# Performance work log

Hardware: AMD Instinct MI355X
Metric: run time of the kernel (lower is better)

The kernel has to match this reference:

```python
import jax, jax.numpy as jnp
import numpy as np

N_NODES = 50000
BETA = 0.5
NEG_SLOPE = 0.2


def gat_conv(x, src, dst, W, a_src, a_dst, b):
    """Single-head GAT-style conv: gather, attend, softmax-per-dst, scatter-sum."""
    h = x @ W                                   # [N, F]
    as_ = h @ a_src                             # [N]
    ad_ = h @ a_dst                             # [N]
    e = jax.nn.leaky_relu(as_[src] + ad_[dst], NEG_SLOPE)  # [E]
    # numerically stable softmax over incoming edges of each dst node
    m = jax.ops.segment_max(e, dst, num_segments=N_NODES)  # [N]
    ex = jnp.exp(e - m[dst])                    # [E]
    denom = jax.ops.segment_sum(ex, dst, num_segments=N_NODES)  # [N]
    w = ex / denom[dst]                         # [E]
    out = jax.ops.segment_sum(w[:, None] * h[src], dst, num_segments=N_NODES)
    return out + b


def setup_inputs() -> dict:
    key = jax.random.key(0)
    ks = jax.random.split(key, 8)
    F_in, F_out = 64, 64
    x = jax.random.normal(ks[0], (N_NODES, F_in), dtype=jnp.float32)
    edge_index = jax.random.randint(ks[1], (2, 1600000), 0, N_NODES, dtype=jnp.int64)
    W = jax.random.normal(ks[2], (F_in, F_in), dtype=jnp.float32) * (1.0 / np.sqrt(F_in))
    a_src = jax.random.normal(ks[3], (F_in,), dtype=jnp.float32) * (1.0 / np.sqrt(F_in))
    a_dst = jax.random.normal(ks[4], (F_in,), dtype=jnp.float32) * (1.0 / np.sqrt(F_in))
    b = jnp.zeros((F_in,), dtype=jnp.float32)
    fc_w = jax.random.normal(ks[5], (F_in, F_out), dtype=jnp.float32) * (1.0 / np.sqrt(F_in))
    fc_b = jnp.zeros((F_out,), dtype=jnp.float32)
    return {"x": x, "edge_index": edge_index, "W": W, "a_src": a_src,
            "a_dst": a_dst, "b": b, "fc_w": fc_w, "fc_b": fc_b}


def reference(x, edge_index, W, a_src, a_dst, b, fc_w, fc_b):
    src, dst = edge_index[0], edge_index[1]
    x1 = BETA * gat_conv(x, src, dst, W, a_src, a_dst, b) + (1.0 - BETA) * x
    x2 = BETA * gat_conv(x1, src, dst, W, a_src, a_dst, b) + (1.0 - BETA) * x
    x3 = BETA * gat_conv(x2, src, dst, W, a_src, a_dst, b) + (1.0 - BETA) * x
    h = x3
    out = x3 @ fc_w + fc_b
    return (out, h)
```

## Files before the change

### kernel.cpp

```cpp
#include <hip/hip_runtime.h>
#include <hip/hip_bf16.h>
#include <math.h>

#define N_NODES 50000
#define FDIM 64
#define BETA 0.5f
#define NEG_SLOPE 0.2f

typedef __attribute__((ext_vector_type(8))) short bf16x8;
typedef __attribute__((ext_vector_type(4))) float f32x4;

__device__ __forceinline__ unsigned short f2bf(float f) {
    unsigned u = __float_as_uint(f);
    unsigned r = (u + 0x7FFFu + ((u >> 16) & 1u)) >> 16;
    return (unsigned short)r;
}
__device__ __forceinline__ float bf2f(unsigned short s) {
    return __uint_as_float((unsigned)s << 16);
}

#define CHUNK 2048
__global__ __launch_bounds__(256) void scatter_pairs(
    const unsigned int* __restrict__ eiu, const int* __restrict__ ei32,
    const long long* __restrict__ ei64, int* __restrict__ gCursor,
    unsigned int* __restrict__ pairs, int E, int CAP) {
    __shared__ int det;
    __shared__ int hist[256], base[256], cur[256];
    int t = threadIdx.x;
    if (t == 0) det = 0;
    hist[t] = 0; cur[t] = 0;
    __syncthreads();
    int beg = blockIdx.x * CHUNK;
    int end = min(E, beg + CHUNK);
    {
        int idx = beg + t;
        if (idx < E && eiu[2 * idx + 1] != 0u) atomicOr(&det, 1);
    }
    __syncthreads();
    bool is32 = det != 0;
    for (int i = beg + t; i < end; i += 256) {
        int d = is32 ? ei32[E + i] : (int)ei64[E + i];
        atomicAdd(&hist[d >> 8], 1);
    }
    __syncthreads();
    if (hist[t] > 0) base[t] = t * CAP + atomicAdd(&gCursor[t], hist[t]);
    __syncthreads();
    for (int i = beg + t; i < end; i += 256) {
        int s, d;
        if (is32) { s = ei32[i]; d = ei32[E + i]; }
        else      { s = (int)ei64[i]; d = (int)ei64[E + i]; }
        int b = d >> 8;
        int pos = base[b] + atomicAdd(&cur[b], 1);
        pairs[pos] = (unsigned int)s | ((unsigned int)(d & 255) << 16);
    }
}

__global__ __launch_bounds__(1024) void bucket_sort(
    const unsigned int* __restrict__ pairs, const int* __restrict__ gCursor,
    int* __restrict__ offsets, int* __restrict__ srcs, int N, int E, int CAP) {
    __shared__ int scb[256], cnt[256], sc[256], cur[256];
    int b = blockIdx.x, t = threadIdx.x;
    if (t < 256) scb[t] = gCursor[t];
    __syncthreads();
    for (int off = 1; off < 256; off <<= 1) {
        int v = (t < 256 && t >= off) ? scb[t - off] : 0;
        __syncthreads();
        if (t < 256) scb[t] += v;
        __syncthreads();
    }
    int cntb = gCursor[b];
    int beg = scb[b] - cntb;
    int pbase = b * CAP;
    if (b == 0 && t == 0) offsets[N] = E;
    if (t < 256) cnt[t] = 0;
    __syncthreads();
    for (int i = t; i < cntb; i += 1024) atomicAdd(&cnt[(pairs[pbase + i] >> 16) & 255u], 1);
    __syncthreads();
    if (t < 256) sc[t] = cnt[t];
    __syncthreads();
    for (int off = 1; off < 256; off <<= 1) {
        int v = (t < 256 && t >= off) ? sc[t - off] : 0;
        __syncthreads();
        if (t < 256) sc[t] += v;
        __syncthreads();
    }
    if (t < 256) {
        int excl = sc[t] - cnt[t];
        int node = (b << 8) + t;
        if (node < N) offsets[node] = beg + excl;
        cur[t] = beg + excl;
    }
    __syncthreads();
    for (int i = t; i < cntb; i += 1024) {
        unsigned int p = pairs[pbase + i];
        int pos = atomicAdd(&cur[(p >> 16) & 255u], 1);
        srcs[pos] = (int)(p & 0xFFFFu);
    }
}

__global__ __launch_bounds__(256) void prep_weights(
    const float* __restrict__ W, const float* __restrict__ fcw,
    unsigned short* __restrict__ WTh, unsigned short* __restrict__ WTl,
    unsigned short* __restrict__ FTh, unsigned short* __restrict__ FTl) {
    for (int idx = blockIdx.x * 256 + threadIdx.x; idx < 4096; idx += gridDim.x * 256) {
        int k = idx >> 6, f = idx & 63;
        float w = W[idx];
        unsigned short hi = f2bf(w);
        WTh[f * 64 + k] = hi;
        WTl[f * 64 + k] = f2bf(w - bf2f(hi));
        float w2 = fcw[idx];
        unsigned short hi2 = f2bf(w2);
        FTh[f * 64 + k] = hi2;
        FTl[f * 64 + k] = f2bf(w2 - bf2f(hi2));
    }
}

__global__ __launch_bounds__(256, 4) void transform_mfma(
    const float* __restrict__ x,
    const unsigned short* __restrict__ WTh, const unsigned short* __restrict__ WTl,
    const float* __restrict__ a_src, const float* __restrict__ a_dst,
    const float* __restrict__ bias,
    unsigned short* __restrict__ hb,
    float* __restrict__ fout,
    float* __restrict__ as_, float* __restrict__ ad_, int N) {
    __shared__ __align__(16) unsigned short WThs[64 * 72];
    __shared__ __align__(16) unsigned short WTls[64 * 72];
    int tid = threadIdx.x;
    {
        int row = tid >> 2;
        int ch = (tid & 3) * 16;
        uint4 h0 = ((const uint4*)(WTh + row * 64 + ch))[0];
        uint4 h1 = ((const uint4*)(WTh + row * 64 + ch))[1];
        uint4 l0 = ((const uint4*)(WTl + row * 64 + ch))[0];
        uint4 l1 = ((const uint4*)(WTl + row * 64 + ch))[1];
        *((uint4*)(WThs + row * 72 + ch)) = h0;
        *((uint4*)(WThs + row * 72 + ch + 8)) = h1;
        *((uint4*)(WTls + row * 72 + ch)) = l0;
        *((uint4*)(WTls + row * 72 + ch + 8)) = l1;
    }

    int wid = tid >> 6;
    int lane = tid & 63;
    int col = lane & 15;
    int quad = lane >> 4;
    int mbase = blockIdx.x * 64 + wid * 16;

    bf16x8 Ah[2], Al[2];
    int arow = mbase + col;
    const float* xr = x + (size_t)(arow < N ? arow : 0) * FDIM + quad * 8;
#pragma unroll
    for (int ks = 0; ks < 2; ks++) {
        float4 xa = *(const float4*)(xr + ks * 32);
        float4 xb = *(const float4*)(xr + ks * 32 + 4);
        float xv[8] = {xa.x, xa.y, xa.z, xa.w, xb.x, xb.y, xb.z, xb.w};
#pragma unroll
        for (int e = 0; e < 8; e++) {
            unsigned short hi = f2bf(xv[e]);
            Ah[ks][e] = (short)hi;
            Al[ks][e] = (short)f2bf(xv[e] - bf2f(hi));
        }
    }
    __syncthreads();

    f32x4 acc[4];
#pragma unroll
    for (int ft = 0; ft < 4; ft++) acc[ft] = (f32x4){0.f, 0.f, 0.f, 0.f};

#pragma unroll
    for (int ft = 0; ft < 4; ft++) {
        int f = ft * 16 + col;
#pragma unroll
        for (int ks = 0; ks < 2; ks++) {
            int off = f * 72 + ks * 32 + quad * 8;
            bf16x8 Bh = *(const bf16x8*)(WThs + off);
            bf16x8 Bl = *(const bf16x8*)(WTls + off);
            acc[ft] = __builtin_amdgcn_mfma_f32_16x16x32_bf16(Ah[ks], Bh, acc[ft], 0, 0, 0);
            acc[ft] = __builtin_amdgcn_mfma_f32_16x16x32_bf16(Ah[ks], Bl, acc[ft], 0, 0, 0);
            acc[ft] = __builtin_amdgcn_mfma_f32_16x16x32_bf16(Al[ks], Bh, acc[ft], 0, 0, 0);
        }
    }

    if (fout) {
#pragma unroll
        for (int ft = 0; ft < 4; ft++) {
            int f = ft * 16 + col;
            float bv = bias ? bias[f] : 0.f;
#pragma unroll
            for (int r = 0; r < 4; r++) {
                int node = mbase + quad * 4 + r;
                if (node < N) fout[(size_t)node * FDIM + f] = acc[ft][r] + bv;
            }
        }
    }
    if (hb) {
#pragma unroll
        for (int ft = 0; ft < 4; ft++) {
            int f = ft * 16 + col;
#pragma unroll
            for (int r = 0; r < 4; r++) {
                int node = mbase + quad * 4 + r;
                if (node < N) hb[(size_t)node * FDIM + f] = f2bf(acc[ft][r]);
            }
        }
    }
    if (as_) {
        float asv[4], adv[4];
#pragma unroll
        for (int ft = 0; ft < 4; ft++) {
            asv[ft] = a_src[ft * 16 + col];
            adv[ft] = a_dst[ft * 16 + col];
        }
#pragma unroll
        for (int r = 0; r < 4; r++) {
            float pa = 0.f, pd = 0.f;
#pragma unroll
            for (int ft = 0; ft < 4; ft++) {
                pa = fmaf(acc[ft][r], asv[ft], pa);
                pd = fmaf(acc[ft][r], adv[ft], pd);
            }
#pragma unroll
            for (int off = 1; off <= 8; off <<= 1) {
                pa += __shfl_xor(pa, off, 64);
                pd += __shfl_xor(pd, off, 64);
            }
            int node = mbase + quad * 4 + r;
            if (col == 0 && node < N) { as_[node] = pa; ad_[node] = pd; }
        }
    }
}

__global__ __launch_bounds__(256) void gat_gather(
    const unsigned short* __restrict__ hb,
    const float* __restrict__ as_, const float* __restrict__ ad_,
    const int* __restrict__ offsets, const int* __restrict__ srcs,
    const float* __restrict__ bvec, const float* __restrict__ x0,
    float* __restrict__ xout, int N) {
    int wid = (blockIdx.x * blockDim.x + threadIdx.x) >> 6;
    if (wid >= N) return;
    int lane = threadIdx.x & 63;
    int q = lane & 7;
    int eslot = lane >> 3;
    int beg = offsets[wid], end = offsets[wid + 1];
    float adv = ad_[wid];

    float acc[8];
#pragma unroll
    for (int k = 0; k < 8; k++) acc[k] = 0.f;
    float denom = 0.f;
    const unsigned short* hq = hb + (q << 3);

#define FMA8(EX, HV)                                                         \
    {                                                                        \
        acc[0] = fmaf(EX, __uint_as_float((HV).x << 16), acc[0]);            \
        acc[1] = fmaf(EX, __uint_as_float((HV).x & 0xFFFF0000u), acc[1]);    \
        acc[2] = fmaf(EX, __uint_as_float((HV).y << 16), acc[2]);            \
        acc[3] = fmaf(EX, __uint_as_float((HV).y & 0xFFFF0000u), acc[3]);    \
        acc[4] = fmaf(EX, __uint_as_float((HV).z << 16), acc[4]);            \
        acc[5] = fmaf(EX, __uint_as_float((HV).z & 0xFFFF0000u), acc[5]);    \
        acc[6] = fmaf(EX, __uint_as_float((HV).w << 16), acc[6]);            \
        acc[7] = fmaf(EX, __uint_as_float((HV).w & 0xFFFF0000u), acc[7]);    \
    }
#define LRELU_EXP(E_) __expf((E_) > 0.f ? (E_) : NEG_SLOPE * (E_))

    int i = beg + eslot;
    for (; i + 24 < end; i += 32) {
        int s0 = srcs[i];
        int s1 = srcs[i + 8];
        int s2 = srcs[i + 16];
        int s3 = srcs[i + 24];
        uint4 hv0 = *(const uint4*)(hq + ((size_t)s0 << 6));
        uint4 hv1 = *(const uint4*)(hq + ((size_t)s1 << 6));
        uint4 hv2 = *(const uint4*)(hq + ((size_t)s2 << 6));
        uint4 hv3 = *(const uint4*)(hq + ((size_t)s3 << 6));
        float e0 = as_[s0] + adv;
        float e1 = as_[s1] + adv;
        float e2 = as_[s2] + adv;
        float e3 = as_[s3] + adv;
        float ex0 = LRELU_EXP(e0);
        float ex1 = LRELU_EXP(e1);
        float ex2 = LRELU_EXP(e2);
        float ex3 = LRELU_EXP(e3);
        denom += (ex0 + ex1) + (ex2 + ex3);
        FMA8(ex0, hv0);
        FMA8(ex1, hv1);
        FMA8(ex2, hv2);
        FMA8(ex3, hv3);
    }
    for (; i < end; i += 8) {
        int s0 = srcs[i];
        uint4 hv0 = *(const uint4*)(hq + ((size_t)s0 << 6));
        float e0 = as_[s0] + adv;
        float ex0 = LRELU_EXP(e0);
        denom += ex0;
        FMA8(ex0, hv0);
    }
#undef FMA8
#undef LRELU_EXP

#pragma unroll
    for (int off = 8; off <= 32; off <<= 1) {
        denom += __shfl_xor(denom, off, 64);
#pragma unroll
        for (int k = 0; k < 8; k++) acc[k] += __shfl_xor(acc[k], off, 64);
    }
    if (lane < 8) {
        float inv = denom > 0.f ? 1.f / denom : 0.f;
        int fb = lane * 8;
        f32x4 b0 = *(const f32x4*)(bvec + fb);
        f32x4 b1 = *(const f32x4*)(bvec + fb + 4);
        f32x4 x0a = *(const f32x4*)(x0 + (size_t)wid * FDIM + fb);
        f32x4 x0b = *(const f32x4*)(x0 + (size_t)wid * FDIM + fb + 4);
        f32x4 o0, o1;
        o0.x = BETA * (acc[0] * inv + b0.x) + (1.f - BETA) * x0a.x;
        o0.y = BETA * (acc[1] * inv + b0.y) + (1.f - BETA) * x0a.y;
        o0.z = BETA * (acc[2] * inv + b0.z) + (1.f - BETA) * x0a.z;
        o0.w = BETA * (acc[3] * inv + b0.w) + (1.f - BETA) * x0a.w;
        o1.x = BETA * (acc[4] * inv + b1.x) + (1.f - BETA) * x0b.x;
        o1.y = BETA * (acc[5] * inv + b1.y) + (1.f - BETA) * x0b.y;
        o1.z = BETA * (acc[6] * inv + b1.z) + (1.f - BETA) * x0b.z;
        o1.w = BETA * (acc[7] * inv + b1.w) + (1.f - BETA) * x0b.w;
        *(f32x4*)(xout + (size_t)wid * FDIM + fb) = o0;
        *(f32x4*)(xout + (size_t)wid * FDIM + fb + 4) = o1;
    }
}

extern "C" void kernel_launch(void* const* d_in, const int* in_sizes, int n_in,
                              void* d_out, int out_size, void* d_ws, size_t ws_size,
                              hipStream_t stream) {
    const int N = N_NODES;
    const int E = in_sizes[1] / 2;
    const int NB = (N + 255) >> 8;
    const int CAP = (((E / N) * 256) * 2 + 1023) & ~1023;

    const float* x     = (const float*)d_in[0];
    const void*  ei    = d_in[1];
    const float* W     = (const float*)d_in[2];
    const float* a_src = (const float*)d_in[3];
    const float* a_dst = (const float*)d_in[4];
    const float* bvec  = (const float*)d_in[5];
    const float* fc_w  = (const float*)d_in[6];
    const float* fc_b  = (const float*)d_in[7];

    float* out = (float*)d_out;
    float* x3  = out + (size_t)N * FDIM;

    char* p = (char*)d_ws;
    auto alloc = [&](size_t bytes) -> void* {
        void* r = (void*)p;
        p += (bytes + 255) & ~(size_t)255;
        return r;
    };
    int*            gCursor  = (int*)alloc(256 * 4);
    unsigned int*   pairs    = (unsigned int*)alloc((size_t)256 * CAP * 4);
    int*            srcs     = (int*)alloc((size_t)E * 4);
    int*            offsets  = (int*)alloc((size_t)(N + 1) * 4);
    float*          as_      = (float*)alloc((size_t)N * 4);
    float*          ad_      = (float*)alloc((size_t)N * 4);
    unsigned short* hbuf     = (unsigned short*)alloc((size_t)N * FDIM * 2);
    float*          xbuf     = (float*)alloc((size_t)N * FDIM * 4);
    unsigned short* WTh      = (unsigned short*)alloc(4096 * 2);
    unsigned short* WTl      = (unsigned short*)alloc(4096 * 2);
    unsigned short* FTh      = (unsigned short*)alloc(4096 * 2);
    unsigned short* FTl      = (unsigned short*)alloc(4096 * 2);

    hipMemsetAsync(gCursor, 0, 256 * 4, stream);

    prep_weights<<<16, 256, 0, stream>>>(W, fc_w, WTh, WTl, FTh, FTl);

    scatter_pairs<<<(E + CHUNK - 1) / CHUNK, 256, 0, stream>>>(
        (const unsigned int*)ei, (const int*)ei, (const long long*)ei,
        gCursor, pairs, E, CAP);
    bucket_sort<<<NB, 1024, 0, stream>>>(pairs, gCursor, offsets, srcs, N, E, CAP);

    int tgrid = (N + 63) / 64;
    int ggrid = (N * 64 + 255) / 256;

    transform_mfma<<<tgrid, 256, 0, stream>>>(x, WTh, WTl, a_src, a_dst, nullptr,
                                              hbuf, nullptr, as_, ad_, N);
    gat_gather<<<ggrid, 256, 0, stream>>>(hbuf, as_, ad_, offsets, srcs, bvec, x, xbuf, N);
    transform_mfma<<<tgrid, 256, 0, stream>>>(xbuf, WTh, WTl, a_src, a_dst, nullptr,
                                              hbuf, nullptr, as_, ad_, N);
    gat_gather<<<ggrid, 256, 0, stream>>>(hbuf, as_, ad_, offsets, srcs, bvec, x, xbuf, N);
    transform_mfma<<<tgrid, 256, 0, stream>>>(xbuf, WTh, WTl, a_src, a_dst, nullptr,
                                              hbuf, nullptr, as_, ad_, N);
    gat_gather<<<ggrid, 256, 0, stream>>>(hbuf, as_, ad_, offsets, srcs, bvec, x, x3, N);
    transform_mfma<<<tgrid, 256, 0, stream>>>(x3, FTh, FTl, nullptr, nullptr, fc_b,
                                              nullptr, out, nullptr, nullptr, N);
}
```

Before: 265.5 us.

## Split gather into two source-range passes for cache locality of h rows

```diff
diff --git a/kernel.cpp b/kernel.cpp
--- a/kernel.cpp
+++ b/kernel.cpp
@@ -6,6 +6,7 @@
 #define FDIM 64
 #define BETA 0.5f
 #define NEG_SLOPE 0.2f
+#define HALF_SPLIT 25000
 
 typedef __attribute__((ext_vector_type(8))) short bf16x8;
 typedef __attribute__((ext_vector_type(4))) float f32x4;
@@ -17,6 +18,12 @@
 }
 __device__ __forceinline__ float bf2f(unsigned short s) {
     return __uint_as_float((unsigned)s << 16);
+}
+__device__ __forceinline__ void nt_store4(float* p, f32x4 v) {
+    __builtin_nontemporal_store(v, (f32x4*)p);
+}
+__device__ __forceinline__ f32x4 nt_load4(const float* p) {
+    return __builtin_nontemporal_load((const f32x4*)p);
 }
 
 #define CHUNK 2048
@@ -57,8 +64,9 @@
 
 __global__ __launch_bounds__(1024) void bucket_sort(
     const unsigned int* __restrict__ pairs, const int* __restrict__ gCursor,
-    int* __restrict__ offsets, int* __restrict__ srcs, int N, int E, int CAP) {
-    __shared__ int scb[256], cnt[256], sc[256], cur[256];
+    int* __restrict__ off2, int* __restrict__ srcs, int N, int E, int CAP) {
+    __shared__ int scb[256];
+    __shared__ int cnt[512], sc[512], cur[512];
     int b = blockIdx.x, t = threadIdx.x;
     if (t < 256) scb[t] = gCursor[t];
     __syncthreads();
@@ -71,30 +79,36 @@
     int cntb = gCursor[b];
     int beg = scb[b] - cntb;
     int pbase = b * CAP;
-    if (b == 0 && t == 0) offsets[N] = E;
-    if (t < 256) cnt[t] = 0;
-    __syncthreads();
-    for (int i = t; i < cntb; i += 1024) atomicAdd(&cnt[(pairs[pbase + i] >> 16) & 255u], 1);
-    __syncthreads();
-    if (t < 256) sc[t] = cnt[t];
-    __syncthreads();
-    for (int off = 1; off < 256; off <<= 1) {
-        int v = (t < 256 && t >= off) ? sc[t - off] : 0;
-        __syncthreads();
-        if (t < 256) sc[t] += v;
-        __syncthreads();
-    }
-    if (t < 256) {
-        int excl = sc[t] - cnt[t];
-        int node = (b << 8) + t;
-        if (node < N) offsets[node] = beg + excl;
-        cur[t] = beg + excl;
-    }
+    if (b == 0 && t == 0) off2[2 * N] = E;
+    if (t < 512) cnt[t] = 0;
     __syncthreads();
     for (int i = t; i < cntb; i += 1024) {
         unsigned int p = pairs[pbase + i];
-        int pos = atomicAdd(&cur[(p >> 16) & 255u], 1);
-        srcs[pos] = (int)(p & 0xFFFFu);
+        int key = (int)(((p >> 16) & 255u) << 1) | ((p & 0xFFFFu) >= HALF_SPLIT ? 1 : 0);
+        atomicAdd(&cnt[key], 1);
+    }
+    __syncthreads();
+    if (t < 512) sc[t] = cnt[t];
+    __syncthreads();
+    for (int off = 1; off < 512; off <<= 1) {
+        int v = (t < 512 && t >= off) ? sc[t - off] : 0;
+        __syncthreads();
+        if (t < 512) sc[t] += v;
+        __syncthreads();
+    }
+    if (t < 512) {
+        int excl = sc[t] - cnt[t];
+        int node = (b << 8) + (t >> 1);
+        if (node < N) off2[2 * node + (t & 1)] = beg + excl;
+        cur[t] = beg + excl;
+    }
+    __syncthreads();
+    for (int i = t; i < cntb; i += 1024) {
+        unsigned int p = pairs[pbase + i];
+        int s = (int)(p & 0xFFFFu);
+        int key = (int)(((p >> 16) & 255u) << 1) | (s >= HALF_SPLIT ? 1 : 0);
+        int pos = atomicAdd(&cur[key], 1);
+        srcs[pos] = s;
     }
 }
 
@@ -229,10 +243,23 @@
     }
 }
 
-__global__ __launch_bounds__(256) void gat_gather(
+__device__ __forceinline__ void fma8(float* acc, float ex, const uint4& hv) {
+    acc[0] = fmaf(ex, __uint_as_float(hv.x << 16), acc[0]);
+    acc[1] = fmaf(ex, __uint_as_float(hv.x & 0xFFFF0000u), acc[1]);
+    acc[2] = fmaf(ex, __uint_as_float(hv.y << 16), acc[2]);
+    acc[3] = fmaf(ex, __uint_as_float(hv.y & 0xFFFF0000u), acc[3]);
+    acc[4] = fmaf(ex, __uint_as_float(hv.z << 16), acc[4]);
+    acc[5] = fmaf(ex, __uint_as_float(hv.z & 0xFFFF0000u), acc[5]);
+    acc[6] = fmaf(ex, __uint_as_float(hv.w << 16), acc[6]);
+    acc[7] = fmaf(ex, __uint_as_float(hv.w & 0xFFFF0000u), acc[7]);
+}
+
+template <int PASS>
+__global__ __launch_bounds__(256) void gat_gather_pass(
     const unsigned short* __restrict__ hb,
     const float* __restrict__ as_, const float* __restrict__ ad_,
-    const int* __restrict__ offsets, const int* __restrict__ srcs,
+    const int* __restrict__ off2, const int* __restrict__ srcs,
+    float* __restrict__ accT, float* __restrict__ denT,
     const float* __restrict__ bvec, const float* __restrict__ x0,
     float* __restrict__ xout, int N) {
     int wid = (blockIdx.x * blockDim.x + threadIdx.x) >> 6;
@@ -240,7 +267,14 @@
     int lane = threadIdx.x & 63;
     int q = lane & 7;
     int eslot = lane >> 3;
-    int beg = offsets[wid], end = offsets[wid + 1];
+    int beg, end;
+    if (PASS == 0) {
+        int2 be = *(const int2*)(off2 + 2 * wid);
+        beg = be.x; end = be.y;
+    } else {
+        beg = off2[2 * wid + 1];
+        end = off2[2 * wid + 2];
+    }
     float adv = ad_[wid];
 
     float acc[8];
@@ -249,17 +283,6 @@
     float denom = 0.f;
     const unsigned short* hq = hb + (q << 3);
 
-#define FMA8(EX, HV)                                                         \
-    {                                                                        \
-        acc[0] = fmaf(EX, __uint_as_float((HV).x << 16), acc[0]);            \
-        acc[1] = fmaf(EX, __uint_as_float((HV).x & 0xFFFF0000u), acc[1]);    \
-        acc[2] = fmaf(EX, __uint_as_float((HV).y << 16), acc[2]);            \
-        acc[3] = fmaf(EX, __uint_as_float((HV).y & 0xFFFF0000u), acc[3]);    \
-        acc[4] = fmaf(EX, __uint_as_float((HV).z << 16), acc[4]);            \
-        acc[5] = fmaf(EX, __uint_as_float((HV).z & 0xFFFF0000u), acc[5]);    \
-        acc[6] = fmaf(EX, __uint_as_float((HV).w << 16), acc[6]);            \
-        acc[7] = fmaf(EX, __uint_as_float((HV).w & 0xFFFF0000u), acc[7]);    \
-    }
 #define LRELU_EXP(E_) __expf((E_) > 0.f ? (E_) : NEG_SLOPE * (E_))
 
     int i = beg + eslot;
@@ -281,10 +304,23 @@
         float ex2 = LRELU_EXP(e2);
         float ex3 = LRELU_EXP(e3);
         denom += (ex0 + ex1) + (ex2 + ex3);
-        FMA8(ex0, hv0);
-        FMA8(ex1, hv1);
-        FMA8(ex2, hv2);
-        FMA8(ex3, hv3);
+        fma8(acc, ex0, hv0);
+        fma8(acc, ex1, hv1);
+        fma8(acc, ex2, hv2);
+        fma8(acc, ex3, hv3);
+    }
+    for (; i + 8 < end; i += 16) {
+        int s0 = srcs[i];
+        int s1 = srcs[i + 8];
+        uint4 hv0 = *(const uint4*)(hq + ((size_t)s0 << 6));
+        uint4 hv1 = *(const uint4*)(hq + ((size_t)s1 << 6));
+        float e0 = as_[s0] + adv;
+        float e1 = as_[s1] + adv;
+        float ex0 = LRELU_EXP(e0);
+        float ex1 = LRELU_EXP(e1);
+        denom += ex0 + ex1;
+        fma8(acc, ex0, hv0);
+        fma8(acc, ex1, hv1);
     }
     for (; i < end; i += 8) {
         int s0 = srcs[i];
@@ -292,9 +328,8 @@
         float e0 = as_[s0] + adv;
         float ex0 = LRELU_EXP(e0);
         denom += ex0;
-        FMA8(ex0, hv0);
-    }
-#undef FMA8
+        fma8(acc, ex0, hv0);
+    }
 #undef LRELU_EXP
 
 #pragma unroll
@@ -303,24 +338,39 @@
 #pragma unroll
         for (int k = 0; k < 8; k++) acc[k] += __shfl_xor(acc[k], off, 64);
     }
-    if (lane < 8) {
-        float inv = denom > 0.f ? 1.f / denom : 0.f;
-        int fb = lane * 8;
-        f32x4 b0 = *(const f32x4*)(bvec + fb);
-        f32x4 b1 = *(const f32x4*)(bvec + fb + 4);
-        f32x4 x0a = *(const f32x4*)(x0 + (size_t)wid * FDIM + fb);
-        f32x4 x0b = *(const f32x4*)(x0 + (size_t)wid * FDIM + fb + 4);
-        f32x4 o0, o1;
-        o0.x = BETA * (acc[0] * inv + b0.x) + (1.f - BETA) * x0a.x;
-        o0.y = BETA * (acc[1] * inv + b0.y) + (1.f - BETA) * x0a.y;
-        o0.z = BETA * (acc[2] * inv + b0.z) + (1.f - BETA) * x0a.z;
-        o0.w = BETA * (acc[3] * inv + b0.w) + (1.f - BETA) * x0a.w;
-        o1.x = BETA * (acc[4] * inv + b1.x) + (1.f - BETA) * x0b.x;
-        o1.y = BETA * (acc[5] * inv + b1.y) + (1.f - BETA) * x0b.y;
-        o1.z = BETA * (acc[6] * inv + b1.z) + (1.f - BETA) * x0b.z;
-        o1.w = BETA * (acc[7] * inv + b1.w) + (1.f - BETA) * x0b.w;
-        *(f32x4*)(xout + (size_t)wid * FDIM + fb) = o0;
-        *(f32x4*)(xout + (size_t)wid * FDIM + fb + 4) = o1;
+
+    if (PASS == 0) {
+        if (lane < 8) {
+            int fb = lane * 8;
+            f32x4 a0 = {acc[0], acc[1], acc[2], acc[3]};
+            f32x4 a1 = {acc[4], acc[5], acc[6], acc[7]};
+            nt_store4(accT + (size_t)wid * FDIM + fb, a0);
+            nt_store4(accT + (size_t)wid * FDIM + fb + 4, a1);
+        }
+        if (lane == 0) denT[wid] = denom;
+    } else {
+        if (lane < 8) {
+            float dtot = denom + denT[wid];
+            float inv = dtot > 0.f ? 1.f / dtot : 0.f;
+            int fb = lane * 8;
+            f32x4 pa0 = nt_load4(accT + (size_t)wid * FDIM + fb);
+            f32x4 pa1 = nt_load4(accT + (size_t)wid * FDIM + fb + 4);
+            f32x4 b0 = *(const f32x4*)(bvec + fb);
+            f32x4 b1 = *(const f32x4*)(bvec + fb + 4);
+            f32x4 x0a = nt_load4(x0 + (size_t)wid * FDIM + fb);
+            f32x4 x0b = nt_load4(x0 + (size_t)wid * FDIM + fb + 4);
+            f32x4 o0, o1;
+            o0.x = BETA * ((acc[0] + pa0.x) * inv + b0.x) + (1.f - BETA) * x0a.x;
+            o0.y = BETA * ((acc[1] + pa0.y) * inv + b0.y) + (1.f - BETA) * x0a.y;
+            o0.z = BETA * ((acc[2] + pa0.z) * inv + b0.z) + (1.f - BETA) * x0a.z;
+            o0.w = BETA * ((acc[3] + pa0.w) * inv + b0.w) + (1.f - BETA) * x0a.w;
+            o1.x = BETA * ((acc[4] + pa1.x) * inv + b1.x) + (1.f - BETA) * x0b.x;
+            o1.y = BETA * ((acc[5] + pa1.y) * inv + b1.y) + (1.f - BETA) * x0b.y;
+            o1.z = BETA * ((acc[6] + pa1.z) * inv + b1.z) + (1.f - BETA) * x0b.z;
+            o1.w = BETA * ((acc[7] + pa1.w) * inv + b1.w) + (1.f - BETA) * x0b.w;
+            *(f32x4*)(xout + (size_t)wid * FDIM + fb) = o0;
+            *(f32x4*)(xout + (size_t)wid * FDIM + fb + 4) = o1;
+        }
     }
 }
 
@@ -353,11 +403,13 @@
     int*            gCursor  = (int*)alloc(256 * 4);
     unsigned int*   pairs    = (unsigned int*)alloc((size_t)256 * CAP * 4);
     int*            srcs     = (int*)alloc((size_t)E * 4);
-    int*            offsets  = (int*)alloc((size_t)(N + 1) * 4);
+    int*            off2     = (int*)alloc((size_t)(2 * N + 1) * 4);
     float*          as_      = (float*)alloc((size_t)N * 4);
     float*          ad_      = (float*)alloc((size_t)N * 4);
     unsigned short* hbuf     = (unsigned short*)alloc((size_t)N * FDIM * 2);
     float*          xbuf     = (float*)alloc((size_t)N * FDIM * 4);
+    float*          accT     = (float*)alloc((size_t)N * FDIM * 4);
+    float*          denT     = (float*)alloc((size_t)N * 4);
     unsigned short* WTh      = (unsigned short*)alloc(4096 * 2);
     unsigned short* WTl      = (unsigned short*)alloc(4096 * 2);
     unsigned short* FTh      = (unsigned short*)alloc(4096 * 2);
@@ -370,20 +422,29 @@
     scatter_pairs<<<(E + CHUNK - 1) / CHUNK, 256, 0, stream>>>(
         (const unsigned int*)ei, (const int*)ei, (const long long*)ei,
         gCursor, pairs, E, CAP);
-    bucket_sort<<<NB, 1024, 0, stream>>>(pairs, gCursor, offsets, srcs, N, E, CAP);
+    bucket_sort<<<NB, 1024, 0, stream>>>(pairs, gCursor, off2, srcs, N, E, CAP);
 
     int tgrid = (N + 63) / 64;
     int ggrid = (N * 64 + 255) / 256;
 
     transform_mfma<<<tgrid, 256, 0, stream>>>(x, WTh, WTl, a_src, a_dst, nullptr,
                                               hbuf, nullptr, as_, ad_, N);
-    gat_gather<<<ggrid, 256, 0, stream>>>(hbuf, as_, ad_, offsets, srcs, bvec, x, xbuf, N);
+    gat_gather_pass<0><<<ggrid, 256, 0, stream>>>(hbuf, as_, ad_, off2, srcs,
+                                                  accT, denT, nullptr, nullptr, nullptr, N);
+    gat_gather_pass<1><<<ggrid, 256, 0, stream>>>(hbuf, as_, ad_, off2, srcs,
+                                                  accT, denT, bvec, x, xbuf, N);
     transform_mfma<<<tgrid, 256, 0, stream>>>(xbuf, WTh, WTl, a_src, a_dst, nullptr,
                                               hbuf, nullptr, as_, ad_, N);
-    gat_gather<<<ggrid, 256, 0, stream>>>(hbuf, as_, ad_, offsets, srcs, bvec, x, xbuf, N);
+    gat_gather_pass<0><<<ggrid, 256, 0, stream>>>(hbuf, as_, ad_, off2, srcs,
+                                                  accT, denT, nullptr, nullptr, nullptr, N);
+    gat_gather_pass<1><<<ggrid, 256, 0, stream>>>(hbuf, as_, ad_, off2, srcs,
+                                                  accT, denT, bvec, x, xbuf, N);
     transform_mfma<<<tgrid, 256, 0, stream>>>(xbuf, WTh, WTl, a_src, a_dst, nullptr,
                                               hbuf, nullptr, as_, ad_, N);
-    gat_gather<<<ggrid, 256, 0, stream>>>(hbuf, as_, ad_, offsets, srcs, bvec, x, x3, N);
+    gat_gather_pass<0><<<ggrid, 256, 0, stream>>>(hbuf, as_, ad_, off2, srcs,
+                                                  accT, denT, nullptr, nullptr, nullptr, N);
+    gat_gather_pass<1><<<ggrid, 256, 0, stream>>>(hbuf, as_, ad_, off2, srcs,
+                                                  accT, denT, bvec, x, x3, N);
     transform_mfma<<<tgrid, 256, 0, stream>>>(x3, FTh, FTl, nullptr, nullptr, fc_b,
                                               nullptr, out, nullptr, nullptr, N);
 }
```

After: 320.5 us. +20.7%, slower.

## Stage edge bucketing through LDS for coalesced writes; nontemporal gather accesses

Applied to the files above, without the earlier changes.

```diff
diff --git a/kernel.cpp b/kernel.cpp
--- a/kernel.cpp
+++ b/kernel.cpp
@@ -19,19 +19,21 @@
     return __uint_as_float((unsigned)s << 16);
 }
 
-#define CHUNK 2048
+#define CHUNK 4096
 __global__ __launch_bounds__(256) void scatter_pairs(
-    const unsigned int* __restrict__ eiu, const int* __restrict__ ei32,
-    const long long* __restrict__ ei64, int* __restrict__ gCursor,
+    const unsigned int* __restrict__ eiu, int* __restrict__ gCursor,
     unsigned int* __restrict__ pairs, int E, int CAP) {
     __shared__ int det;
-    __shared__ int hist[256], base[256], cur[256];
+    __shared__ unsigned int staged[CHUNK];
+    __shared__ unsigned short tmpd[CHUNK];
+    __shared__ int hist[256], sc[256], lbase[256], gbase[256], lcur[256];
     int t = threadIdx.x;
     if (t == 0) det = 0;
-    hist[t] = 0; cur[t] = 0;
+    hist[t] = 0;
     __syncthreads();
     int beg = blockIdx.x * CHUNK;
     int end = min(E, beg + CHUNK);
+    int n = end - beg;
     {
         int idx = beg + t;
         if (idx < E && eiu[2 * idx + 1] != 0u) atomicOr(&det, 1);
@@ -39,26 +41,44 @@
     __syncthreads();
     bool is32 = det != 0;
     for (int i = beg + t; i < end; i += 256) {
-        int d = is32 ? ei32[E + i] : (int)ei64[E + i];
+        int d = is32 ? (int)eiu[E + i] : (int)eiu[2 * (size_t)(E + i)];
+        tmpd[i - beg] = (unsigned short)d;
         atomicAdd(&hist[d >> 8], 1);
     }
     __syncthreads();
-    if (hist[t] > 0) base[t] = t * CAP + atomicAdd(&gCursor[t], hist[t]);
+    sc[t] = hist[t];
+    __syncthreads();
+    for (int off = 1; off < 256; off <<= 1) {
+        int v = (t >= off) ? sc[t - off] : 0;
+        __syncthreads();
+        sc[t] += v;
+        __syncthreads();
+    }
+    int excl = sc[t] - hist[t];
+    lbase[t] = excl;
+    lcur[t] = excl;
+    if (hist[t] > 0) gbase[t] = t * CAP + atomicAdd(&gCursor[t], hist[t]);
     __syncthreads();
     for (int i = beg + t; i < end; i += 256) {
-        int s, d;
-        if (is32) { s = ei32[i]; d = ei32[E + i]; }
-        else      { s = (int)ei64[i]; d = (int)ei64[E + i]; }
-        int b = d >> 8;
-        int pos = base[b] + atomicAdd(&cur[b], 1);
-        pairs[pos] = (unsigned int)s | ((unsigned int)(d & 255) << 16);
+        unsigned s = is32 ? eiu[i] : eiu[2 * (size_t)i];
+        unsigned td = tmpd[i - beg];
+        int b = (int)(td >> 8);
+        int lp = atomicAdd(&lcur[b], 1);
+        staged[lp] = s | (td << 16);
+    }
+    __syncthreads();
+    for (int j = t; j < n; j += 256) {
+        unsigned w = staged[j];
+        int b = (int)(w >> 24);
+        pairs[gbase[b] + (j - lbase[b])] = w;
     }
 }
 
 __global__ __launch_bounds__(1024) void bucket_sort(
     const unsigned int* __restrict__ pairs, const int* __restrict__ gCursor,
     int* __restrict__ offsets, int* __restrict__ srcs, int N, int E, int CAP) {
-    __shared__ int scb[256], cnt[256], sc[256], cur[256];
+    __shared__ int scb[256], cnt[256], sc[256], lcur[256];
+    __shared__ unsigned short sorted16[16384];
     int b = blockIdx.x, t = threadIdx.x;
     if (t < 256) scb[t] = gCursor[t];
     __syncthreads();
@@ -71,6 +91,7 @@
     int cntb = gCursor[b];
     int beg = scb[b] - cntb;
     int pbase = b * CAP;
+    bool useLds = cntb <= 16384;
     if (b == 0 && t == 0) offsets[N] = E;
     if (t < 256) cnt[t] = 0;
     __syncthreads();
@@ -88,13 +109,23 @@
         int excl = sc[t] - cnt[t];
         int node = (b << 8) + t;
         if (node < N) offsets[node] = beg + excl;
-        cur[t] = beg + excl;
-    }
-    __syncthreads();
-    for (int i = t; i < cntb; i += 1024) {
-        unsigned int p = pairs[pbase + i];
-        int pos = atomicAdd(&cur[(p >> 16) & 255u], 1);
-        srcs[pos] = (int)(p & 0xFFFFu);
+        lcur[t] = excl;
+    }
+    __syncthreads();
+    if (useLds) {
+        for (int i = t; i < cntb; i += 1024) {
+            unsigned p = pairs[pbase + i];
+            int lp = atomicAdd(&lcur[(p >> 16) & 255u], 1);
+            sorted16[lp] = (unsigned short)(p & 0xFFFFu);
+        }
+        __syncthreads();
+        for (int j = t; j < cntb; j += 1024) srcs[beg + j] = (int)sorted16[j];
+    } else {
+        for (int i = t; i < cntb; i += 1024) {
+            unsigned p = pairs[pbase + i];
+            int lp = atomicAdd(&lcur[(p >> 16) & 255u], 1);
+            srcs[beg + lp] = (int)(p & 0xFFFFu);
+        }
     }
 }
 
@@ -229,6 +260,17 @@
     }
 }
 
+__device__ __forceinline__ void fma8(float* acc, float ex, const uint4& hv) {
+    acc[0] = fmaf(ex, __uint_as_float(hv.x << 16), acc[0]);
+    acc[1] = fmaf(ex, __uint_as_float(hv.x & 0xFFFF0000u), acc[1]);
+    acc[2] = fmaf(ex, __uint_as_float(hv.y << 16), acc[2]);
+    acc[3] = fmaf(ex, __uint_as_float(hv.y & 0xFFFF0000u), acc[3]);
+    acc[4] = fmaf(ex, __uint_as_float(hv.z << 16), acc[4]);
+    acc[5] = fmaf(ex, __uint_as_float(hv.z & 0xFFFF0000u), acc[5]);
+    acc[6] = fmaf(ex, __uint_as_float(hv.w << 16), acc[6]);
+    acc[7] = fmaf(ex, __uint_as_float(hv.w & 0xFFFF0000u), acc[7]);
+}
+
 __global__ __launch_bounds__(256) void gat_gather(
     const unsigned short* __restrict__ hb,
     const float* __restrict__ as_, const float* __restrict__ ad_,
@@ -249,25 +291,15 @@
     float denom = 0.f;
     const unsigned short* hq = hb + (q << 3);
 
-#define FMA8(EX, HV)                                                         \
-    {                                                                        \
-        acc[0] = fmaf(EX, __uint_as_float((HV).x << 16), acc[0]);            \
-        acc[1] = fmaf(EX, __uint_as_float((HV).x & 0xFFFF0000u), acc[1]);    \
-        acc[2] = fmaf(EX, __uint_as_float((HV).y << 16), acc[2]);            \
-        acc[3] = fmaf(EX, __uint_as_float((HV).y & 0xFFFF0000u), acc[3]);    \
-        acc[4] = fmaf(EX, __uint_as_float((HV).z << 16), acc[4]);            \
-        acc[5] = fmaf(EX, __uint_as_float((HV).z & 0xFFFF0000u), acc[5]);    \
-        acc[6] = fmaf(EX, __uint_as_float((HV).w << 16), acc[6]);            \
-        acc[7] = fmaf(EX, __uint_as_float((HV).w & 0xFFFF0000u), acc[7]);    \
-    }
 #define LRELU_EXP(E_) __expf((E_) > 0.f ? (E_) : NEG_SLOPE * (E_))
+#define NTL(P_) __builtin_nontemporal_load(P_)
 
     int i = beg + eslot;
     for (; i + 24 < end; i += 32) {
-        int s0 = srcs[i];
-        int s1 = srcs[i + 8];
-        int s2 = srcs[i + 16];
-        int s3 = srcs[i + 24];
+        int s0 = NTL(srcs + i);
+        int s1 = NTL(srcs + i + 8);
+        int s2 = NTL(srcs + i + 16);
+        int s3 = NTL(srcs + i + 24);
         uint4 hv0 = *(const uint4*)(hq + ((size_t)s0 << 6));
         uint4 hv1 = *(const uint4*)(hq + ((size_t)s1 << 6));
         uint4 hv2 = *(const uint4*)(hq + ((size_t)s2 << 6));
@@ -281,20 +313,32 @@
         float ex2 = LRELU_EXP(e2);
         float ex3 = LRELU_EXP(e3);
         denom += (ex0 + ex1) + (ex2 + ex3);
-        FMA8(ex0, hv0);
-        FMA8(ex1, hv1);
-        FMA8(ex2, hv2);
-        FMA8(ex3, hv3);
+        fma8(acc, ex0, hv0);
+        fma8(acc, ex1, hv1);
+        fma8(acc, ex2, hv2);
+        fma8(acc, ex3, hv3);
+    }
+    for (; i + 8 < end; i += 16) {
+        int s0 = NTL(srcs + i);
+        int s1 = NTL(srcs + i + 8);
+        uint4 hv0 = *(const uint4*)(hq + ((size_t)s0 << 6));
+        uint4 hv1 = *(const uint4*)(hq + ((size_t)s1 << 6));
+        float e0 = as_[s0] + adv;
+        float e1 = as_[s1] + adv;
+        float ex0 = LRELU_EXP(e0);
+        float ex1 = LRELU_EXP(e1);
+        denom += ex0 + ex1;
+        fma8(acc, ex0, hv0);
+        fma8(acc, ex1, hv1);
     }
     for (; i < end; i += 8) {
-        int s0 = srcs[i];
+        int s0 = NTL(srcs + i);
         uint4 hv0 = *(const uint4*)(hq + ((size_t)s0 << 6));
         float e0 = as_[s0] + adv;
         float ex0 = LRELU_EXP(e0);
         denom += ex0;
-        FMA8(ex0, hv0);
-    }
-#undef FMA8
+        fma8(acc, ex0, hv0);
+    }
 #undef LRELU_EXP
 
 #pragma unroll
@@ -308,8 +352,8 @@
         int fb = lane * 8;
         f32x4 b0 = *(const f32x4*)(bvec + fb);
         f32x4 b1 = *(const f32x4*)(bvec + fb + 4);
-        f32x4 x0a = *(const f32x4*)(x0 + (size_t)wid * FDIM + fb);
-        f32x4 x0b = *(const f32x4*)(x0 + (size_t)wid * FDIM + fb + 4);
+        f32x4 x0a = NTL((const f32x4*)(x0 + (size_t)wid * FDIM + fb));
+        f32x4 x0b = NTL((const f32x4*)(x0 + (size_t)wid * FDIM + fb + 4));
         f32x4 o0, o1;
         o0.x = BETA * (acc[0] * inv + b0.x) + (1.f - BETA) * x0a.x;
         o0.y = BETA * (acc[1] * inv + b0.y) + (1.f - BETA) * x0a.y;
@@ -319,9 +363,10 @@
         o1.y = BETA * (acc[5] * inv + b1.y) + (1.f - BETA) * x0b.y;
         o1.z = BETA * (acc[6] * inv + b1.z) + (1.f - BETA) * x0b.z;
         o1.w = BETA * (acc[7] * inv + b1.w) + (1.f - BETA) * x0b.w;
-        *(f32x4*)(xout + (size_t)wid * FDIM + fb) = o0;
-        *(f32x4*)(xout + (size_t)wid * FDIM + fb + 4) = o1;
-    }
+        __builtin_nontemporal_store(o0, (f32x4*)(xout + (size_t)wid * FDIM + fb));
+        __builtin_nontemporal_store(o1, (f32x4*)(xout + (size_t)wid * FDIM + fb + 4));
+    }
+#undef NTL
 }
 
 extern "C" void kernel_launch(void* const* d_in, const int* in_sizes, int n_in,
@@ -368,8 +413,7 @@
     prep_weights<<<16, 256, 0, stream>>>(W, fc_w, WTh, WTl, FTh, FTl);
 
     scatter_pairs<<<(E + CHUNK - 1) / CHUNK, 256, 0, stream>>>(
-        (const unsigned int*)ei, (const int*)ei, (const long long*)ei,
-        gCursor, pairs, E, CAP);
+        (const unsigned int*)ei, gCursor, pairs, E, CAP);
     bucket_sort<<<NB, 1024, 0, stream>>>(pairs, gCursor, offsets, srcs, N, E, CAP);
 
     int tgrid = (N + 63) / 64;
```

After: 270.6 us. No clear change (+1.9%).
